# Kernel tuning notes

Hardware: AMD Instinct MI355X
Metric: run time of the kernel (lower is better)

Reference implementation:

```python
import jax, jax.numpy as jnp
import numpy as np

B, S, D = 8, 1025, 768
H, KV, HD = 12, 4, 64
GH, GW = 32, 32
EPS = 1e-6


def setup_inputs() -> dict:
    key = jax.random.key(0)
    ks = jax.random.split(key, 6)
    sc = 0.02
    hidden_states = jax.random.normal(ks[0], (B, S, D), jnp.float32)
    attention_mask = jnp.ones((B, S), dtype=bool)
    image_pos_ids = jnp.broadcast_to(jnp.arange(S, dtype=jnp.int32), (B, S))
    return dict(
        hidden_states=hidden_states,
        attention_mask=attention_mask,
        image_pos_ids=image_pos_ids,
        grid_h=GH,
        grid_w=GW,
        Wq=jax.random.normal(ks[1], (D, H * HD), jnp.float32) * sc,
        Wk=jax.random.normal(ks[2], (D, KV * HD), jnp.float32) * sc,
        Wv=jax.random.normal(ks[3], (D, KV * HD), jnp.float32) * sc,
        Wo=jax.random.normal(ks[4], (H * HD, D), jnp.float32) * sc,
        q_norm_w=jnp.ones((HD,), jnp.float32),
        k_norm_w=jnp.ones((HD,), jnp.float32),
    )


def _rmsnorm(x, w, eps=EPS):
    return x * jax.lax.rsqrt(jnp.mean(x * x, axis=-1, keepdims=True) + eps) * w


def _rotate(x, cos, sin):
    # x: [B, h, P, HD]; cos/sin: [B, P, HD//2]. Pairs are adjacent (view_as_complex).
    hd = x.shape[-1]
    xr = x.reshape(*x.shape[:-1], hd // 2, 2)
    x0, x1 = xr[..., 0], xr[..., 1]
    c, s = cos[:, None], sin[:, None]  # broadcast over heads
    o0 = x0 * c - x1 * s
    o1 = x0 * s + x1 * c
    return jnp.stack([o0, o1], axis=-1).reshape(x.shape)


def reference(hidden_states, attention_mask, image_pos_ids, grid_h, grid_w,
              Wq, Wk, Wv, Wo, q_norm_w, k_norm_w):
    b, s, d = hidden_states.shape
    hd = q_norm_w.shape[0]
    h = Wq.shape[1] // hd
    kv = Wk.shape[1] // hd
    n_rep = h // kv
    scale = hd ** -0.5

    q = _rmsnorm((hidden_states @ Wq).reshape(b, s, h, hd), q_norm_w).transpose(0, 2, 1, 3)
    k = _rmsnorm((hidden_states @ Wk).reshape(b, s, kv, hd), k_norm_w).transpose(0, 2, 1, 3)
    v = (hidden_states @ Wv).reshape(b, s, kv, hd).transpose(0, 2, 1, 3)

    # 2D RoPE on patch tokens only (CLS token at position 0 excluded)
    ids = image_pos_ids[:, 1:]
    hi = (ids // grid_w) % grid_h
    wi = ids % grid_w
    half, quarter = hd // 2, hd // 4
    inv_freq = 1.0 / (10000.0 ** (jnp.arange(quarter, dtype=jnp.float32) * 2.0 / half))
    ang = jnp.concatenate([hi[..., None] * inv_freq, wi[..., None] * inv_freq], axis=-1)  # [B,P,HD/2]
    cos, sin = jnp.cos(ang), jnp.sin(ang)
    q = jnp.concatenate([q[:, :, :1], _rotate(q[:, :, 1:], cos, sin)], axis=2)
    k = jnp.concatenate([k[:, :, :1], _rotate(k[:, :, 1:], cos, sin)], axis=2)

    # GQA: repeat_interleave kv heads to match query heads
    kr = jnp.repeat(k, n_rep, axis=1)
    vr = jnp.repeat(v, n_rep, axis=1)

    scores = jnp.einsum('bhqd,bhkd->bhqk', q, kr) * scale
    add = jnp.where(attention_mask, 0.0, jnp.finfo(jnp.float32).min)[:, None, None, :]
    scores = scores + add
    attn = jax.nn.softmax(scores.astype(jnp.float32), axis=-1).astype(q.dtype)
    out = jnp.einsum('bhqk,bhkd->bqhd', attn, vr).reshape(b, s, h * hd)
    return (out @ Wo, attn)
```

## Files before the change

kernel.cpp:

```cpp
#include <hip/hip_runtime.h>

#define B_ 8
#define S_ 1025
#define D_ 768
#define H_ 12
#define KV_ 4
#define HD_ 64
#define NREP 3
#define SCALE_ 0.125f
#define EPS_ 1e-6f
#define SKP 1088
#define SCS 1092
#define QBLK 16
#define NQT 65

typedef __attribute__((ext_vector_type(8))) short bf16x8;
typedef __attribute__((ext_vector_type(4))) float f32x4;

__device__ __forceinline__ unsigned short f2bf(float f) {
  unsigned int u = __builtin_bit_cast(unsigned int, f);
  return (unsigned short)((u + 0x7FFFu + ((u >> 16) & 1u)) >> 16);
}
__device__ __forceinline__ unsigned int pk2(float a, float b) {
  return (unsigned int)f2bf(a) | ((unsigned int)f2bf(b) << 16);
}

__global__ __launch_bounds__(256) void cast_x_kernel(const float* __restrict__ x,
                                                     unsigned short* __restrict__ xb, int n4) {
  int i = blockIdx.x * 256 + threadIdx.x;
  if (i >= n4) return;
  f32x4 v = *(const f32x4*)(x + (size_t)i * 4);
  uint2 o;
  o.x = pk2(v[0], v[1]);
  o.y = pk2(v[2], v[3]);
  *(uint2*)(xb + (size_t)i * 4) = o;
}

__global__ __launch_bounds__(256) void cast_wqkv_kernel(const float* __restrict__ Wq,
    const float* __restrict__ Wk, const float* __restrict__ Wv,
    unsigned short* __restrict__ WT) {
  int idx = blockIdx.x * 256 + threadIdx.x;
  int n = idx / D_, k = idx % D_;
  float v;
  if (n < 768)       v = Wq[(size_t)k * 768 + n];
  else if (n < 1024) v = Wk[(size_t)k * 256 + (n - 768)];
  else               v = Wv[(size_t)k * 256 + (n - 1024)];
  WT[idx] = f2bf(v);
}

__global__ __launch_bounds__(256) void cast_wo_kernel(const float* __restrict__ Wo,
                                                      unsigned short* __restrict__ WT) {
  int idx = blockIdx.x * 256 + threadIdx.x;
  int n = idx / D_, k = idx % D_;
  WT[idx] = f2bf(Wo[(size_t)k * D_ + n]);
}

#define BM 128
#define BN 128
#define BK 32
#define LSTR 40
__global__ __launch_bounds__(256) void gemm_bt(const unsigned short* __restrict__ A,
    const unsigned short* __restrict__ BT, float* __restrict__ C, int M, int N, int K) {
  __shared__ unsigned short As[BM * LSTR];
  __shared__ unsigned short Bs[BN * LSTR];
  const int nMt = (M + BM - 1) / BM;
  const int tm = blockIdx.x % nMt;
  const int tn = blockIdx.x / nMt;
  const int row0 = tm * BM, col0 = tn * BN;
  const int tid = threadIdx.x;
  const int l = tid & 63, w = tid >> 6;
  const int wr = (w >> 1) * 64, wc = (w & 1) * 64;
  const int lr = l & 15, lk = (l >> 4) * 8;
  f32x4 acc[4][4] = {};
  for (int kt = 0; kt < K; kt += BK) {
    __syncthreads();
#pragma unroll
    for (int i = 0; i < 2; ++i) {
      int c = tid + i * 256;
      int r = c >> 2;
      int ce = (c & 3) * 8;
      int gr = row0 + r; gr = gr < M ? gr : M - 1;
      bf16x8 va = *(const bf16x8*)(A + (size_t)gr * K + kt + ce);
      *(bf16x8*)&As[r * LSTR + ce] = va;
      bf16x8 vb = *(const bf16x8*)(BT + (size_t)(col0 + r) * K + kt + ce);
      *(bf16x8*)&Bs[r * LSTR + ce] = vb;
    }
    __syncthreads();
    bf16x8 af[4], bfr[4];
#pragma unroll
    for (int m = 0; m < 4; ++m)
      af[m] = *(const bf16x8*)&As[(wr + m * 16 + lr) * LSTR + lk];
#pragma unroll
    for (int n = 0; n < 4; ++n)
      bfr[n] = *(const bf16x8*)&Bs[(wc + n * 16 + lr) * LSTR + lk];
#pragma unroll
    for (int m = 0; m < 4; ++m)
#pragma unroll
      for (int n = 0; n < 4; ++n)
        acc[m][n] = __builtin_amdgcn_mfma_f32_16x16x32_bf16(af[m], bfr[n], acc[m][n], 0, 0, 0);
  }
  const int orow = (l >> 4) * 4;
#pragma unroll
  for (int m = 0; m < 4; ++m)
#pragma unroll
    for (int n = 0; n < 4; ++n)
#pragma unroll
      for (int r = 0; r < 4; ++r) {
        int row = row0 + wr + m * 16 + orow + r;
        int col = col0 + wc + n * 16 + lr;
        if (row < M) C[(size_t)row * N + col] = acc[m][n][r];
      }
}

__global__ __launch_bounds__(256) void qkv_epilogue(const float* __restrict__ QKV,
    const int* __restrict__ pos_ids, const int* __restrict__ ghp, const int* __restrict__ gwp,
    const float* __restrict__ qw, const float* __restrict__ kw,
    unsigned short* __restrict__ Qb, unsigned short* __restrict__ Kb,
    unsigned short* __restrict__ Vt) {
  int tok = blockIdx.x * 4 + (threadIdx.x >> 6);
  int l = threadIdx.x & 63;
  if (tok >= B_ * S_) return;
  int b = tok / S_, s = tok % S_;
  const float* rowp = QKV + (size_t)tok * 1280;
  bool rot = (s > 0);
  float cs = 1.f, sn = 0.f;
  if (rot) {
    int gh = ghp[0], gw = gwp[0];
    int pos = pos_ids[tok];
    int hi = (pos / gw) % gh;
    int wi = pos % gw;
    int pi = l >> 1;
    int j = pi < 16 ? pi : pi - 16;
    float invf = exp2f(-(float)j * (13.287712379549449f / 16.f));
    float ang = (pi < 16 ? (float)hi : (float)wi) * invf;
    cs = cosf(ang); sn = sinf(ang);
  }
#pragma unroll
  for (int h = 0; h < H_; ++h) {
    float x = rowp[h * 64 + l];
    float ss = x * x;
    for (int off = 32; off; off >>= 1) ss += __shfl_xor(ss, off);
    float xn = x * rsqrtf(ss * (1.f / 64.f) + EPS_) * qw[l];
    float o = xn;
    if (rot) {
      float p = __shfl_xor(xn, 1);
      o = (l & 1) ? (p * sn + xn * cs) : (xn * cs - p * sn);
    }
    o *= SCALE_;
    Qb[((size_t)(b * H_ + h) * S_ + s) * 64 + l] = f2bf(o);
  }
#pragma unroll
  for (int h = 0; h < KV_; ++h) {
    float x = rowp[768 + h * 64 + l];
    float ss = x * x;
    for (int off = 32; off; off >>= 1) ss += __shfl_xor(ss, off);
    float xn = x * rsqrtf(ss * (1.f / 64.f) + EPS_) * kw[l];
    float o = xn;
    if (rot) {
      float p = __shfl_xor(xn, 1);
      o = (l & 1) ? (p * sn + xn * cs) : (xn * cs - p * sn);
    }
    Kb[((size_t)(b * KV_ + h) * S_ + s) * 64 + l] = f2bf(o);
    float v = rowp[1024 + h * 64 + l];
    Vt[((size_t)(b * KV_ + h) * 64 + l) * SKP + s] = f2bf(v);
  }
}

__global__ __launch_bounds__(512) void attn_kernel(const unsigned short* __restrict__ Qb,
    const unsigned short* __restrict__ Kb, const unsigned short* __restrict__ Vt,
    unsigned short* __restrict__ ctx, float* __restrict__ attn_out) {
  extern __shared__ float Sc[];
  __shared__ float partial[4][64][4];
  int bid = blockIdx.x;
  int swz = (bid & 7) * 780 + (bid >> 3);
  int qt = swz % NQT;
  int h = (swz / NQT) % H_;
  int b = swz / (NQT * H_);
  int kvh = h / NREP;
  int q0 = qt * QBLK;
  int tid = threadIdx.x;
  int l = tid & 63, w = tid >> 6;
  int lr = l & 15, lk = (l >> 4) * 8;

  const unsigned short* Qbase = Qb + (size_t)(b * H_ + h) * S_ * 64;
  const unsigned short* Kbase = Kb + (size_t)(b * KV_ + kvh) * S_ * 64;
  const unsigned short* Vbase = Vt + (size_t)(b * KV_ + kvh) * 64 * SKP;

  int qrow = q0 + lr; if (qrow >= S_) qrow = S_ - 1;
  bf16x8 qf0 = *(const bf16x8*)(Qbase + (size_t)qrow * 64 + lk);
  bf16x8 qf1 = *(const bf16x8*)(Qbase + (size_t)qrow * 64 + 32 + lk);

  {
    const int kcol = w * 16 + lr;
    const int nT = (w < 4) ? 9 : 8;
    const unsigned short* kp = Kbase + (size_t)kcol * 64;
    bf16x8 kf0 = *(const bf16x8*)(kp + lk);
    bf16x8 kf1 = *(const bf16x8*)(kp + 32 + lk);
    for (int t = 0; t < nT; ++t) {
      bf16x8 nf0 = kf0, nf1 = kf1;
      if (t + 1 < nT) {
        int kr = (t + 1) * 128 + kcol; if (kr >= S_) kr = S_ - 1;
        const unsigned short* np = Kbase + (size_t)kr * 64;
        nf0 = *(const bf16x8*)(np + lk);
        nf1 = *(const bf16x8*)(np + 32 + lk);
      }
      f32x4 acc = {};
      acc = __builtin_amdgcn_mfma_f32_16x16x32_bf16(qf0, kf0, acc, 0, 0, 0);
      acc = __builtin_amdgcn_mfma_f32_16x16x32_bf16(qf1, kf1, acc, 0, 0, 0);
      int col = t * 128 + kcol;
      int rowb = (l >> 4) * 4;
#pragma unroll
      for (int r = 0; r < 4; ++r) Sc[(size_t)(rowb + r) * SCS + col] = acc[r];
      kf0 = nf0; kf1 = nf1;
    }
  }
  __syncthreads();

#pragma unroll
  for (int rr = 0; rr < 2; ++rr) {
    int rowi = w + rr * 8;
    int q = q0 + rowi;
    float* srow = Sc + (size_t)rowi * SCS;
    float vals[17];
    float mx = -1e30f;
#pragma unroll
    for (int i = 0; i < 17; ++i) {
      int key = l + i * 64;
      float v = (key < S_) ? srow[key] : -1e30f;
      vals[i] = v;
      mx = fmaxf(mx, v);
    }
    for (int off = 32; off; off >>= 1) mx = fmaxf(mx, __shfl_xor(mx, off));
    float sum = 0.f;
#pragma unroll
    for (int i = 0; i < 17; ++i) {
      float e = __expf(vals[i] - mx);
      vals[i] = e; sum += e;
    }
    for (int off = 32; off; off >>= 1) sum += __shfl_xor(sum, off);
    float inv = 1.f / sum;
    if (q < S_) {
      float* gout = attn_out + ((size_t)(b * H_ + h) * S_ + q) * S_;
#pragma unroll
      for (int i = 0; i < 17; ++i) {
        int key = l + i * 64;
        if (key < S_) __builtin_nontemporal_store(vals[i] * inv, gout + key);
      }
    }
    unsigned short* urow = (unsigned short*)srow;
#pragma unroll
    for (int i = 0; i < 17; ++i) {
      int key = l + i * 64;
      float p = (key < S_) ? vals[i] * inv : 0.f;
      urow[key] = f2bf(p);
    }
  }
  __syncthreads();

  f32x4 accv = {};
  {
    const int d0 = (w & 3) * 16;
    const int kh = (w >> 2) * 544;
    const unsigned short* U = (const unsigned short*)Sc;
    const int prow = lr * (SCS * 2);
    const unsigned short* vb = Vbase + (size_t)(d0 + lr) * SKP + kh;
#pragma unroll 4
    for (int kc = 0; kc < 17; ++kc) {
      bf16x8 pa = *(const bf16x8*)&U[prow + kh + kc * 32 + lk];
      bf16x8 vf = *(const bf16x8*)(vb + kc * 32 + lk);
      accv = __builtin_amdgcn_mfma_f32_16x16x32_bf16(pa, vf, accv, 0, 0, 0);
    }
  }
  if (w >= 4) *(f32x4*)partial[w - 4][l] = accv;
  __syncthreads();
  if (w < 4) {
    accv += *(const f32x4*)partial[w][l];
    int rowb = (l >> 4) * 4;
    int d0 = (w & 3) * 16;
#pragma unroll
    for (int r = 0; r < 4; ++r) {
      int q = q0 + rowb + r;
      if (q < S_)
        ctx[(size_t)(b * S_ + q) * 768 + h * 64 + d0 + lr] = f2bf(accv[r]);
    }
  }
}

extern "C" void kernel_launch(void* const* d_in, const int* in_sizes, int n_in,
                              void* d_out, int out_size, void* d_ws, size_t ws_size,
                              hipStream_t stream) {
  const float* hidden = (const float*)d_in[0];
  const int* pos_ids = (const int*)d_in[2];
  const int* ghp = (const int*)d_in[3];
  const int* gwp = (const int*)d_in[4];
  const float* Wq = (const float*)d_in[5];
  const float* Wk = (const float*)d_in[6];
  const float* Wv = (const float*)d_in[7];
  const float* Wo = (const float*)d_in[8];
  const float* qnw = (const float*)d_in[9];
  const float* knw = (const float*)d_in[10];

  char* ws = (char*)d_ws;
  unsigned short* Xb    = (unsigned short*)ws;
  unsigned short* WqkvT = (unsigned short*)(ws + 12595200);
  unsigned short* WoT   = (unsigned short*)(ws + 14561280);
  float*          QKV   = (float*)(ws + 15740928);
  unsigned short* ctx   = (unsigned short*)(ws + 15740928);
  unsigned short* Qb    = (unsigned short*)(ws + 57724928);
  unsigned short* Kb    = (unsigned short*)(ws + 70320128);
  unsigned short* Vt    = (unsigned short*)(ws + 74518528);

  float* out0 = (float*)d_out;
  float* attn_out = out0 + (size_t)B_ * S_ * D_;

  cast_x_kernel<<<6150, 256, 0, stream>>>(hidden, Xb, 1574400);
  cast_wqkv_kernel<<<3840, 256, 0, stream>>>(Wq, Wk, Wv, WqkvT);
  cast_wo_kernel<<<2304, 256, 0, stream>>>(Wo, WoT);

  gemm_bt<<<65 * 10, 256, 0, stream>>>(Xb, WqkvT, QKV, B_ * S_, 1280, D_);

  hipMemsetAsync(Vt, 0, 4456448, stream);
  qkv_epilogue<<<2050, 256, 0, stream>>>(QKV, pos_ids, ghp, gwp, qnw, knw, Qb, Kb, Vt);

  hipFuncSetAttribute((const void*)attn_kernel,
                      hipFuncAttributeMaxDynamicSharedMemorySize, QBLK * SCS * 4);
  attn_kernel<<<B_ * H_ * NQT, 512, QBLK * SCS * 4, stream>>>(Qb, Kb, Vt, ctx, attn_out);

  gemm_bt<<<65 * 6, 256, 0, stream>>>(ctx, WoT, out0, B_ * S_, D_, D_);
}
```

Baseline: 351.9 us.

## Defer attention-prob stores and compact bf16 P buffer in LDS

Softmax probabilities for both rows are kept in registers, then written as bf16 into a compact LDS buffer with a new stride, after an extra barrier that keeps the float score reads from racing with the writes. The global fp32 attention-matrix stores are moved to the end of the kernel, after the PV MFMA and the ctx write, so they can overlap with the rest of the work instead of stalling before PV. Launch bounds now ask for 4 blocks per CU. The tail-store loop is simplified to 16 full chunks plus one lane. The costs are higher register pressure from holding 34 values per thread, which the occupancy hint may turn into spills, and one added barrier.

```diff
diff --git a/kernel.cpp b/kernel.cpp
--- a/kernel.cpp
+++ b/kernel.cpp
@@ -11,6 +11,7 @@
 #define EPS_ 1e-6f
 #define SKP 1088
 #define SCS 1092
+#define PST 1096
 #define QBLK 16
 #define NQT 65
 
@@ -166,7 +167,7 @@
   }
 }
 
-__global__ __launch_bounds__(512) void attn_kernel(const unsigned short* __restrict__ Qb,
+__global__ __launch_bounds__(512, 4) void attn_kernel(const unsigned short* __restrict__ Qb,
     const unsigned short* __restrict__ Kb, const unsigned short* __restrict__ Vt,
     unsigned short* __restrict__ ctx, float* __restrict__ attn_out) {
   extern __shared__ float Sc[];
@@ -216,43 +217,44 @@
   }
   __syncthreads();
 
+  float vals[2][17];
 #pragma unroll
   for (int rr = 0; rr < 2; ++rr) {
     int rowi = w + rr * 8;
-    int q = q0 + rowi;
-    float* srow = Sc + (size_t)rowi * SCS;
-    float vals[17];
+    const float* srow = Sc + (size_t)rowi * SCS;
     float mx = -1e30f;
 #pragma unroll
     for (int i = 0; i < 17; ++i) {
       int key = l + i * 64;
       float v = (key < S_) ? srow[key] : -1e30f;
-      vals[i] = v;
+      vals[rr][i] = v;
       mx = fmaxf(mx, v);
     }
     for (int off = 32; off; off >>= 1) mx = fmaxf(mx, __shfl_xor(mx, off));
     float sum = 0.f;
 #pragma unroll
     for (int i = 0; i < 17; ++i) {
-      float e = __expf(vals[i] - mx);
-      vals[i] = e; sum += e;
+      float e = __expf(vals[rr][i] - mx);
+      vals[rr][i] = e; sum += e;
     }
     for (int off = 32; off; off >>= 1) sum += __shfl_xor(sum, off);
     float inv = 1.f / sum;
-    if (q < S_) {
-      float* gout = attn_out + ((size_t)(b * H_ + h) * S_ + q) * S_;
-#pragma unroll
-      for (int i = 0; i < 17; ++i) {
-        int key = l + i * 64;
-        if (key < S_) __builtin_nontemporal_store(vals[i] * inv, gout + key);
-      }
-    }
-    unsigned short* urow = (unsigned short*)srow;
 #pragma unroll
     for (int i = 0; i < 17; ++i) {
       int key = l + i * 64;
-      float p = (key < S_) ? vals[i] * inv : 0.f;
-      urow[key] = f2bf(p);
+      vals[rr][i] = (key < S_) ? vals[rr][i] * inv : 0.f;
+    }
+  }
+  __syncthreads();
+
+  {
+    unsigned short* P = (unsigned short*)Sc;
+#pragma unroll
+    for (int rr = 0; rr < 2; ++rr) {
+      int rowi = w + rr * 8;
+      unsigned short* prow = P + (size_t)rowi * PST;
+#pragma unroll
+      for (int i = 0; i < 17; ++i) prow[l + i * 64] = f2bf(vals[rr][i]);
     }
   }
   __syncthreads();
@@ -262,7 +264,7 @@
     const int d0 = (w & 3) * 16;
     const int kh = (w >> 2) * 544;
     const unsigned short* U = (const unsigned short*)Sc;
-    const int prow = lr * (SCS * 2);
+    const int prow = lr * PST;
     const unsigned short* vb = Vbase + (size_t)(d0 + lr) * SKP + kh;
 #pragma unroll 4
     for (int kc = 0; kc < 17; ++kc) {
@@ -282,6 +284,18 @@
       int q = q0 + rowb + r;
       if (q < S_)
         ctx[(size_t)(b * S_ + q) * 768 + h * 64 + d0 + lr] = f2bf(accv[r]);
+    }
+  }
+
+#pragma unroll
+  for (int rr = 0; rr < 2; ++rr) {
+    int q = q0 + w + rr * 8;
+    if (q < S_) {
+      float* gout = attn_out + ((size_t)(b * H_ + h) * S_ + q) * S_;
+#pragma unroll
+      for (int i = 0; i < 16; ++i)
+        __builtin_nontemporal_store(vals[rr][i], gout + l + i * 64);
+      if (l == 0) __builtin_nontemporal_store(vals[rr][16], gout + 1024);
     }
   }
 }
```

Measured after the change: 354.8 us. No clear change (+0.8%).

## Store attention scores as fp16 in LDS to halve shared memory footprint

Applied to the files above, without the earlier changes.

The score tile in LDS is stored as fp16 instead of fp32, roughly halving dynamic shared memory so more attention blocks fit per CU (launch bounds now request 8 waves-per-EU occupancy). The separate memset of the V-transpose padding is replaced by zeroing only the padded columns inside the epilogue kernel, and the barriers become explicit lgkm waits plus s_barrier. The bf16 probability rows use a padded, row-staggered layout to reduce bank conflicts. Storing scores in fp16 loses some precision before the softmax and could overflow for large logits.

```diff
diff --git a/kernel.cpp b/kernel.cpp
--- a/kernel.cpp
+++ b/kernel.cpp
@@ -1,4 +1,5 @@
 #include <hip/hip_runtime.h>
+#include <hip/hip_fp16.h>
 
 #define B_ 8
 #define S_ 1025
@@ -10,9 +11,12 @@
 #define SCALE_ 0.125f
 #define EPS_ 1e-6f
 #define SKP 1088
-#define SCS 1092
+#define HSS 1092
 #define QBLK 16
 #define NQT 65
+#define DYNLDS 34944
+
+#define PROW(r) ((r) * HSS + 4 * ((r) & 1))
 
 typedef __attribute__((ext_vector_type(8))) short bf16x8;
 typedef __attribute__((ext_vector_type(4))) float f32x4;
@@ -23,6 +27,13 @@
 }
 __device__ __forceinline__ unsigned int pk2(float a, float b) {
   return (unsigned int)f2bf(a) | ((unsigned int)f2bf(b) << 16);
+}
+
+__device__ __forceinline__ void barrier_lgkm() {
+  __builtin_amdgcn_sched_barrier(0);
+  asm volatile("s_waitcnt lgkmcnt(0)" ::: "memory");
+  __builtin_amdgcn_s_barrier();
+  __builtin_amdgcn_sched_barrier(0);
 }
 
 __global__ __launch_bounds__(256) void cast_x_kernel(const float* __restrict__ x,
@@ -117,6 +128,13 @@
     const float* __restrict__ qw, const float* __restrict__ kw,
     unsigned short* __restrict__ Qb, unsigned short* __restrict__ Kb,
     unsigned short* __restrict__ Vt) {
+  if (blockIdx.x < B_ * KV_) {
+    unsigned short* vp = Vt + (size_t)blockIdx.x * 64 * SKP;
+    for (int idx = threadIdx.x; idx < 64 * 63; idx += 256) {
+      int d = idx / 63, s = S_ + idx % 63;
+      vp[d * SKP + s] = 0;
+    }
+  }
   int tok = blockIdx.x * 4 + (threadIdx.x >> 6);
   int l = threadIdx.x & 63;
   if (tok >= B_ * S_) return;
@@ -166,10 +184,10 @@
   }
 }
 
-__global__ __launch_bounds__(512) void attn_kernel(const unsigned short* __restrict__ Qb,
+__global__ __launch_bounds__(512, 8) void attn_kernel(const unsigned short* __restrict__ Qb,
     const unsigned short* __restrict__ Kb, const unsigned short* __restrict__ Vt,
     unsigned short* __restrict__ ctx, float* __restrict__ attn_out) {
-  extern __shared__ float Sc[];
+  extern __shared__ unsigned short Ush[];
   __shared__ float partial[4][64][4];
   int bid = blockIdx.x;
   int swz = (bid & 7) * 780 + (bid >> 3);
@@ -210,69 +228,70 @@
       int col = t * 128 + kcol;
       int rowb = (l >> 4) * 4;
 #pragma unroll
-      for (int r = 0; r < 4; ++r) Sc[(size_t)(rowb + r) * SCS + col] = acc[r];
+      for (int r = 0; r < 4; ++r)
+        Ush[(size_t)(rowb + r) * HSS + col] =
+            __builtin_bit_cast(unsigned short, __float2half(acc[r]));
       kf0 = nf0; kf1 = nf1;
     }
   }
-  __syncthreads();
+  barrier_lgkm();
 
 #pragma unroll
   for (int rr = 0; rr < 2; ++rr) {
     int rowi = w + rr * 8;
     int q = q0 + rowi;
-    float* srow = Sc + (size_t)rowi * SCS;
-    float vals[17];
+    const unsigned short* Hrow = Ush + (size_t)rowi * HSS;
+    float f[17];
     float mx = -1e30f;
 #pragma unroll
     for (int i = 0; i < 17; ++i) {
       int key = l + i * 64;
-      float v = (key < S_) ? srow[key] : -1e30f;
-      vals[i] = v;
+      float v = (key < S_) ? __half2float(__builtin_bit_cast(__half, Hrow[key])) : -1e30f;
+      f[i] = v;
       mx = fmaxf(mx, v);
     }
     for (int off = 32; off; off >>= 1) mx = fmaxf(mx, __shfl_xor(mx, off));
     float sum = 0.f;
 #pragma unroll
     for (int i = 0; i < 17; ++i) {
-      float e = __expf(vals[i] - mx);
-      vals[i] = e; sum += e;
+      float e = __expf(f[i] - mx);
+      f[i] = e; sum += e;
     }
     for (int off = 32; off; off >>= 1) sum += __shfl_xor(sum, off);
     float inv = 1.f / sum;
+#pragma unroll
+    for (int i = 0; i < 17; ++i) f[i] *= inv;
     if (q < S_) {
       float* gout = attn_out + ((size_t)(b * H_ + h) * S_ + q) * S_;
 #pragma unroll
-      for (int i = 0; i < 17; ++i) {
-        int key = l + i * 64;
-        if (key < S_) __builtin_nontemporal_store(vals[i] * inv, gout + key);
-      }
-    }
-    unsigned short* urow = (unsigned short*)srow;
+      for (int i = 0; i < 16; ++i)
+        __builtin_nontemporal_store(f[i], gout + l + i * 64);
+      if (l == 0) __builtin_nontemporal_store(f[16], gout + 1024);
+    }
+    unsigned short* Prow = Ush + PROW(rowi);
 #pragma unroll
     for (int i = 0; i < 17; ++i) {
       int key = l + i * 64;
-      float p = (key < S_) ? vals[i] * inv : 0.f;
-      urow[key] = f2bf(p);
-    }
-  }
-  __syncthreads();
+      Prow[key] = f2bf((key < S_) ? f[i] : 0.f);
+    }
+  }
+  barrier_lgkm();
 
   f32x4 accv = {};
   {
     const int d0 = (w & 3) * 16;
     const int kh = (w >> 2) * 544;
-    const unsigned short* U = (const unsigned short*)Sc;
-    const int prow = lr * (SCS * 2);
+    const int prow = PROW(lr);
     const unsigned short* vb = Vbase + (size_t)(d0 + lr) * SKP + kh;
 #pragma unroll 4
     for (int kc = 0; kc < 17; ++kc) {
-      bf16x8 pa = *(const bf16x8*)&U[prow + kh + kc * 32 + lk];
+      bf16x8 pa = *(const bf16x8*)&Ush[prow + kh + kc * 32 + lk];
       bf16x8 vf = *(const bf16x8*)(vb + kc * 32 + lk);
       accv = __builtin_amdgcn_mfma_f32_16x16x32_bf16(pa, vf, accv, 0, 0, 0);
     }
   }
   if (w >= 4) *(f32x4*)partial[w - 4][l] = accv;
-  __syncthreads();
+  barrier_lgkm();
   if (w < 4) {
     accv += *(const f32x4*)partial[w][l];
     int rowb = (l >> 4) * 4;
@@ -319,12 +338,11 @@
 
   gemm_bt<<<65 * 10, 256, 0, stream>>>(Xb, WqkvT, QKV, B_ * S_, 1280, D_);
 
-  hipMemsetAsync(Vt, 0, 4456448, stream);
   qkv_epilogue<<<2050, 256, 0, stream>>>(QKV, pos_ids, ghp, gwp, qnw, knw, Qb, Kb, Vt);
 
   hipFuncSetAttribute((const void*)attn_kernel,
-                      hipFuncAttributeMaxDynamicSharedMemorySize, QBLK * SCS * 4);
-  attn_kernel<<<B_ * H_ * NQT, 512, QBLK * SCS * 4, stream>>>(Qb, Kb, Vt, ctx, attn_out);
+                      hipFuncAttributeMaxDynamicSharedMemorySize, DYNLDS);
+  attn_kernel<<<B_ * H_ * NQT, 512, DYNLDS, stream>>>(Qb, Kb, Vt, ctx, attn_out);
 
   gemm_bt<<<65 * 6, 256, 0, stream>>>(ctx, WoT, out0, B_ * S_, D_, D_);
 }
```

New measurement: 335.9 us. 1.05x faster.
